# Performance work log

Hardware: AMD Instinct MI355X
Metric: run time of the kernel (lower is better)

## Reference

```python
import jax, jax.numpy as jnp
import numpy as np

B = 4096
D = 68 * 68  # 4624
L = 68
E = 1024


def setup_inputs() -> dict:
    key = jax.random.key(0)
    ks = jax.random.split(key, 24)
    rn = lambda k, shape, scale: jax.random.normal(k, shape, dtype=jnp.float32) * scale
    inp = {
        "x": rn(ks[0], (B, D), 1.0),
        "eps": rn(ks[1], (B, L), 1.0),
        # weights scaled ~1/sqrt(fan_in) to avoid sigmoid saturation
        "fc11_w": rn(ks[2], (E, D), 1.0 / np.sqrt(D)),
        "fc11_b": rn(ks[3], (E,), 0.01),
        "fc12_w": rn(ks[4], (E, D), 1.0 / np.sqrt(D)),
        "fc12_b": rn(ks[5], (E,), 0.01),
        "fc21_w": rn(ks[6], (L, E), 1.0 / np.sqrt(E)),
        "fc21_b": rn(ks[7], (L,), 0.01),
        "fc22_w": rn(ks[8], (L, E), 1.0 / np.sqrt(E)),
        "fc22_b": rn(ks[9], (L,), 0.01),
        "W3": rn(ks[10], (5, L, L), 1.0 / np.sqrt(L)),
        "b3": rn(ks[11], (5, L), 0.01),
        "W4": rn(ks[12], (5, L, L), 1.0 / np.sqrt(L)),
        "b4": rn(ks[13], (5, L), 0.01),
        "W5": rn(ks[14], (3, L, L), 1.0 / np.sqrt(L)),
        "b5": rn(ks[15], (3, L), 0.01),
        "fc6_w": rn(ks[16], (D, D), 1.0 / np.sqrt(D)),
        "fc6_b": rn(ks[17], (D,), 0.01),
        "fcy_w": rn(ks[18], (1, L), 1.0 / np.sqrt(L)),
        "fcy_b": rn(ks[19], (1,), 0.01),
    }
    return inp


def _forward(x, eps, fc11_w, fc11_b, fc12_w, fc12_b, fc21_w, fc21_b,
             fc22_w, fc22_b, W3, b3, W4, b4, W5, b5, fc6_w, fc6_b, fcy_w, fcy_b):
    b = x.shape[0]
    # encode (dropout in eval mode -> identity)
    h11 = jax.nn.relu(x @ fc11_w.T + fc11_b)
    h12 = jax.nn.relu(x @ fc12_w.T + fc12_b)
    mu = h11 @ fc21_w.T + fc21_b          # [B, 68]
    logvar = h12 @ fc22_w.T + fc22_b      # [B, 68]
    # reparameterize
    z = mu + eps * jnp.exp(0.5 * logvar)
    y = mu @ fcy_w.T + fcy_b              # [B, 1]
    # decode: 5 parallel 68-dim branches (vectorized over branch axis k)
    h3 = jnp.einsum('bd,kod->kbo', z, W3) + b3[:, None, :]     # [5,B,68]
    # source: h31 has no sigmoid, h32..h35 do
    h3 = jnp.concatenate([h3[:1], jax.nn.sigmoid(h3[1:])], axis=0)
    h4 = jax.nn.sigmoid(jnp.einsum('kbd,kod->kbo', h3, W4) + b4[:, None, :])
    # source reuses fc53 for branches 4 and 5: weight index map [0,1,2,2,2]
    idx = jnp.array([0, 1, 2, 2, 2])
    h5 = jnp.einsum('kbd,kod->kbo', h4, W5[idx]) + b5[idx][:, None, :]  # [5,B,68]
    # source: h6 = h51 only (other branch outer-products are dead code)
    h51 = h5[0]                                                # [B,68]
    outer = (h51[:, :, None] * h51[:, None, :]).reshape(b, D)  # bmm outer product
    recon = jax.nn.sigmoid(outer @ fc6_w.T + fc6_b)            # [B, 4624]
    return recon, mu, logvar, y


def reference(x, eps, fc11_w, fc11_b, fc12_w, fc12_b, fc21_w, fc21_b,
              fc22_w, fc22_b, W3, b3, W4, b4, W5, b5, fc6_w, fc6_b, fcy_w, fcy_b):
    return _forward(x, eps, fc11_w, fc11_b, fc12_w, fc12_b, fc21_w, fc21_b,
                    fc22_w, fc22_b, W3, b3, W4, b4, W5, b5, fc6_w, fc6_b, fcy_w, fcy_b)
```

## Files before the change

### kernel.cpp

```cpp
#include <hip/hip_runtime.h>
#include <hip/hip_bf16.h>
#include <cstdint>
#include <cstddef>

typedef __bf16 bf16x8 __attribute__((ext_vector_type(8)));
typedef __bf16 bf16x4 __attribute__((ext_vector_type(4)));
typedef float  floatx4 __attribute__((ext_vector_type(4)));

#define DEV __device__ __forceinline__

DEV __bf16 f2b(float x) { return (__bf16)x; }

DEV void async_ld16(const void* g, void* l) {
    __builtin_amdgcn_global_load_lds(
        (const __attribute__((address_space(1))) unsigned int*)g,
        (__attribute__((address_space(3))) unsigned int*)l,
        16, 0, 0);
}

#define BATCH 4096
#define DDIM  4624
#define DPAD  4672
#define LDIM  68
#define EDIM  1024
#define N1    2048
#define KB    2048
#define N2PAD 4736
#define NPAIR 2346
#define K2PAD 2368

DEV void build_ptab(unsigned short* ptab, int t, int nthr) {
    for (int i = t; i < LDIM; i += nthr) {
        int p0 = i * (137 - i) / 2;
        for (int j = i; j < LDIM; ++j)
            ptab[p0 + (j - i)] = (unsigned short)((i << 8) | j);
    }
}

#define PREP_GRID 7880
__global__ __launch_bounds__(256) void prep(
        const float* __restrict__ x, const float* __restrict__ w11,
        const float* __restrict__ w12, const float* __restrict__ w21,
        const float* __restrict__ w22, const float* __restrict__ w6,
        __bf16* __restrict__ xb, __bf16* __restrict__ w1_pad,
        __bf16* __restrict__ w2_pad, __bf16* __restrict__ w6s) {
    __shared__ float rowbuf[DDIM];
    __shared__ unsigned short ptab[K2PAD];
    const int b = blockIdx.x;
    const int t = threadIdx.x;

    if (b < 3072) {
        const float* src;
        __bf16* dst;
        int rows, lb, vg;
        if (b < 2048)      { src = x;   dst = xb;                          rows = BATCH; lb = b;        vg = 2048; }
        else if (b < 2560) { src = w11; dst = w1_pad;                      rows = 1024;  lb = b - 2048; vg = 512; }
        else               { src = w12; dst = w1_pad + (size_t)1024 * DPAD; rows = 1024; lb = b - 2560; vg = 512; }
        const int gpr = DPAD / 4;
        const long total = (long)rows * gpr;
        for (long g = lb * 256L + t; g < total; g += vg * 256L) {
            int row = (int)(g / gpr);
            int c4  = (int)(g - (long)row * gpr) * 4;
            bf16x4 v;
            if (c4 < DDIM) {
                floatx4 f = *(const floatx4*)(src + (size_t)row * DDIM + c4);
                v[0] = f2b(f[0]); v[1] = f2b(f[1]); v[2] = f2b(f[2]); v[3] = f2b(f[3]);
            } else {
                v[0] = v[1] = v[2] = v[3] = (__bf16)0.0f;
            }
            *(bf16x4*)(dst + (size_t)row * DPAD + c4) = v;
        }
    } else if (b < 3144) {
        const int lb = b - 3072;
        const int total = 144 * 512;
        for (int g = lb * 256 + t; g < total; g += 72 * 256) {
            int row = g >> 9;
            int c4  = (g & 511) * 4;
            bf16x4 v;
            v[0] = v[1] = v[2] = v[3] = (__bf16)0.0f;
            if (row < 68 && c4 < 1024) {
                floatx4 f = *(const floatx4*)(w21 + (size_t)row * EDIM + c4);
                v[0] = f2b(f[0]); v[1] = f2b(f[1]); v[2] = f2b(f[2]); v[3] = f2b(f[3]);
            } else if (row >= 68 && row < 136 && c4 >= 1024) {
                floatx4 f = *(const floatx4*)(w22 + (size_t)(row - 68) * EDIM + (c4 - 1024));
                v[0] = f2b(f[0]); v[1] = f2b(f[1]); v[2] = f2b(f[2]); v[3] = f2b(f[3]);
            }
            *(bf16x4*)(w2_pad + (size_t)row * KB + c4) = v;
        }
    } else {
        const int o = b - 3144;
        if (o < DDIM) {
            const float* src = w6 + (size_t)o * DDIM;
            for (int idx = t; idx < DDIM / 4; idx += 256)
                *(floatx4*)(rowbuf + idx * 4) = *(const floatx4*)(src + idx * 4);
        }
        build_ptab(ptab, t, 256);
        __syncthreads();
        for (int p4 = t; p4 < K2PAD / 4; p4 += 256) {
            bf16x4 v;
#pragma unroll
            for (int u = 0; u < 4; ++u) {
                int p = p4 * 4 + u;
                float val = 0.f;
                if (o < DDIM && p < NPAIR) {
                    int ij = ptab[p];
                    int i = ij >> 8, j = ij & 255;
                    val = (i == j) ? rowbuf[i * LDIM + i]
                                   : (rowbuf[i * LDIM + j] + rowbuf[j * LDIM + i]);
                }
                v[u] = f2b(val);
            }
            *(bf16x4*)(w6s + (size_t)o * K2PAD + p4 * 4) = v;
        }
    }
}

template <int EPI>
__launch_bounds__(256, 2)
__global__ void gemm_bt(const __bf16* __restrict__ A, int lda,
                        const __bf16* __restrict__ W, int ldb, int KT,
                        __bf16* __restrict__ outb, float* __restrict__ outf, int ldc,
                        const float* __restrict__ bias0, const float* __restrict__ bias1) {
    __shared__ __align__(16) __bf16 smA[128 * 64];
    __shared__ __align__(16) __bf16 smB[128 * 64];

    const int t  = threadIdx.x;
    const int l  = t & 63;
    const int w  = t >> 6;
    const int m0 = blockIdx.x * 128;
    const int n0 = blockIdx.y * 128;
    const int wm = (w & 1) * 64;
    const int wn = (w >> 1) * 64;

    const int srow   = t >> 3;
    const int schunk = (t & 7) ^ (srow & 7);
    const __bf16* pa = A + (size_t)(m0 + srow) * lda + schunk * 8;
    const __bf16* pb = W + (size_t)(n0 + srow) * ldb + schunk * 8;
    char* dA = (char*)smA + t * 16;
    char* dB = (char*)smB + t * 16;

    floatx4 acc[4][4];
#pragma unroll
    for (int mi = 0; mi < 4; ++mi)
#pragma unroll
        for (int ni = 0; ni < 4; ++ni) {
            floatx4 z = {0.f, 0.f, 0.f, 0.f};
            acc[mi][ni] = z;
        }

    for (int kt = 0; kt < KT; ++kt) {
#pragma unroll
        for (int i = 0; i < 4; ++i) {
            async_ld16(pa + (size_t)i * 32 * lda, dA + i * 4096);
            async_ld16(pb + (size_t)i * 32 * ldb, dB + i * 4096);
        }
        pa += 64; pb += 64;
        __syncthreads();

#pragma unroll
        for (int h = 0; h < 2; ++h) {
            bf16x8 af[4], bfr[4];
#pragma unroll
            for (int mi = 0; mi < 4; ++mi) {
                int r = wm + mi * 16 + (l & 15);
                int c = ((h << 2) | (l >> 4)) ^ (r & 7);
                af[mi] = *(const bf16x8*)((const char*)smA + r * 128 + c * 16);
            }
#pragma unroll
            for (int ni = 0; ni < 4; ++ni) {
                int r = wn + ni * 16 + (l & 15);
                int c = ((h << 2) | (l >> 4)) ^ (r & 7);
                bfr[ni] = *(const bf16x8*)((const char*)smB + r * 128 + c * 16);
            }
#pragma unroll
            for (int mi = 0; mi < 4; ++mi)
#pragma unroll
                for (int ni = 0; ni < 4; ++ni)
                    acc[mi][ni] = __builtin_amdgcn_mfma_f32_16x16x32_bf16(af[mi], bfr[ni],
                                                                         acc[mi][ni], 0, 0, 0);
        }
        __syncthreads();
    }

    const int colbase = n0 + wn + (l & 15);
    const int rowbase = m0 + wm + (l >> 4) * 4;
#pragma unroll
    for (int ni = 0; ni < 4; ++ni) {
        int col = colbase + ni * 16;
        if (EPI == 1 && col >= DDIM) continue;
        float bias = (EPI == 0)
                         ? ((col < 1024) ? bias0[col] : bias1[col - 1024])
                         : bias0[col];
#pragma unroll
        for (int mi = 0; mi < 4; ++mi) {
            int row = rowbase + mi * 16;
#pragma unroll
            for (int r = 0; r < 4; ++r) {
                float v = acc[mi][ni][r] + bias;
                if (EPI == 0) {
                    v = v > 0.f ? v : 0.f;
                    outb[(size_t)(row + r) * ldc + col] = f2b(v);
                } else {
                    v = 1.f / (1.f + __expf(-v));
                    outf[(size_t)(row + r) * ldc + col] = v;
                }
            }
        }
    }
}

__launch_bounds__(64, 4)
__global__ void gemmB(const __bf16* __restrict__ h, const __bf16* __restrict__ w2,
                      float* __restrict__ muvar) {
    const int l    = threadIdx.x;
    const int m0   = blockIdx.x * 16;
    const int k0   = blockIdx.y * 512;
    const int row  = l & 15;
    const int quad = l >> 4;
    float* mv = muvar + (size_t)blockIdx.y * BATCH * 136;

    floatx4 acc[9];
#pragma unroll
    for (int ni = 0; ni < 9; ++ni) {
        floatx4 z = {0.f, 0.f, 0.f, 0.f};
        acc[ni] = z;
    }

    const __bf16* ap = h + (size_t)(m0 + row) * KB + k0 + quad * 8;
    for (int kt = 0; kt < 16; ++kt) {
        bf16x8 a = *(const bf16x8*)ap;
        ap += 32;
#pragma unroll
        for (int ni = 0; ni < 9; ++ni) {
            const __bf16* bp = w2 + (size_t)(ni * 16 + row) * KB + k0 + kt * 32 + quad * 8;
            bf16x8 b = *(const bf16x8*)bp;
            acc[ni] = __builtin_amdgcn_mfma_f32_16x16x32_bf16(a, b, acc[ni], 0, 0, 0);
        }
    }
#pragma unroll
    for (int ni = 0; ni < 9; ++ni) {
        int col = ni * 16 + row;
        if (col < 136) {
#pragma unroll
            for (int r = 0; r < 4; ++r) {
                int orow = m0 + quad * 4 + r;
                mv[(size_t)orow * 136 + col] = acc[ni][r];
            }
        }
    }
}

__global__ void decode(const float* __restrict__ muvar, const float* __restrict__ eps,
                       const float* __restrict__ b21, const float* __restrict__ b22,
                       const float* __restrict__ W3, const float* __restrict__ b3,
                       const float* __restrict__ W4, const float* __restrict__ b4,
                       const float* __restrict__ W5, const float* __restrict__ b5,
                       const float* __restrict__ fcyw, const float* __restrict__ fcyb,
                       float* __restrict__ out_mu, float* __restrict__ out_lv,
                       float* __restrict__ out_y, __bf16* __restrict__ A2) {
    __shared__ float w3s[DDIM], w4s[DDIM], w5s[DDIM];
    __shared__ float b3s[LDIM], b4s[LDIM], b5s[LDIM], fys[LDIM];
    __shared__ float zb[16][LDIM], h3b[16][LDIM], h51b[16][LDIM], mub[16][LDIM];
    __shared__ unsigned short ptab[K2PAD];

    const int t  = threadIdx.x;
    const int r0 = blockIdx.x * 16;

    for (int i = t; i < DDIM; i += 256) {
        w3s[i] = W3[i];
        w4s[i] = W4[i];
        w5s[i] = W5[i];
    }
    if (t < LDIM) {
        b3s[t] = b3[t];
        b4s[t] = b4[t];
        b5s[t] = b5[t];
        fys[t] = fcyw[t];
    }
    build_ptab(ptab, t, 256);
    __syncthreads();

    for (int idx = t; idx < 16 * LDIM; idx += 256) {
        int r = idx / LDIM, o = idx - r * LDIM;
        int row = r0 + r;
        float mu = b21[o];
        float lv = b22[o];
#pragma unroll
        for (int s = 0; s < 4; ++s) {
            const float* mv = muvar + (size_t)s * BATCH * 136 + (size_t)row * 136;
            mu += mv[o];
            lv += mv[68 + o];
        }
        float z = mu + eps[(size_t)row * LDIM + o] * __expf(0.5f * lv);
        zb[r][o]  = z;
        mub[r][o] = mu;
        out_mu[(size_t)row * LDIM + o] = mu;
        out_lv[(size_t)row * LDIM + o] = lv;
    }
    __syncthreads();

    if (t < 16) {
        int row = r0 + t;
        float s = fcyb[0];
        for (int o = 0; o < LDIM; ++o)
            s += mub[t][o] * fys[o];
        out_y[row] = s;
    }

    for (int idx = t; idx < 16 * LDIM; idx += 256) {
        int r = idx / LDIM, o = idx - r * LDIM;
        float s = b3s[o];
        for (int d = 0; d < LDIM; ++d) s += zb[r][d] * w3s[o * LDIM + d];
        h3b[r][o] = s;
    }
    __syncthreads();

    for (int idx = t; idx < 16 * LDIM; idx += 256) {
        int r = idx / LDIM, o = idx - r * LDIM;
        float s = b4s[o];
        for (int d = 0; d < LDIM; ++d) s += h3b[r][d] * w4s[o * LDIM + d];
        zb[r][o] = 1.f / (1.f + __expf(-s));
    }
    __syncthreads();

    for (int idx = t; idx < 16 * LDIM; idx += 256) {
        int r = idx / LDIM, o = idx - r * LDIM;
        float s = b5s[o];
        for (int d = 0; d < LDIM; ++d) s += zb[r][d] * w5s[o * LDIM + d];
        h51b[r][o] = s;
    }
    __syncthreads();

    for (int idx = t; idx < 16 * (K2PAD / 4); idx += 256) {
        int r  = idx / (K2PAD / 4);
        int p4 = (idx - r * (K2PAD / 4)) * 4;
        int row = r0 + r;
        bf16x4 v;
#pragma unroll
        for (int u = 0; u < 4; ++u) {
            int p = p4 + u;
            float val = 0.f;
            if (p < NPAIR) {
                int ij = ptab[p];
                val = h51b[r][ij >> 8] * h51b[r][ij & 255];
            }
            v[u] = f2b(val);
        }
        *(bf16x4*)(A2 + (size_t)row * K2PAD + p4) = v;
    }
}

extern "C" void kernel_launch(void* const* d_in, const int* in_sizes, int n_in,
                              void* d_out, int out_size, void* d_ws, size_t ws_size,
                              hipStream_t stream) {
    const float* x    = (const float*)d_in[0];
    const float* eps  = (const float*)d_in[1];
    const float* w11  = (const float*)d_in[2];
    const float* b11  = (const float*)d_in[3];
    const float* w12  = (const float*)d_in[4];
    const float* b12  = (const float*)d_in[5];
    const float* w21  = (const float*)d_in[6];
    const float* b21  = (const float*)d_in[7];
    const float* w22  = (const float*)d_in[8];
    const float* b22  = (const float*)d_in[9];
    const float* W3   = (const float*)d_in[10];
    const float* b3   = (const float*)d_in[11];
    const float* W4   = (const float*)d_in[12];
    const float* b4   = (const float*)d_in[13];
    const float* W5   = (const float*)d_in[14];
    const float* b5   = (const float*)d_in[15];
    const float* w6   = (const float*)d_in[16];
    const float* b6   = (const float*)d_in[17];
    const float* fcyw = (const float*)d_in[18];
    const float* fcyb = (const float*)d_in[19];

    float* out       = (float*)d_out;
    float* out_recon = out;
    float* out_mu    = out + (size_t)BATCH * DDIM;
    float* out_lv    = out_mu + (size_t)BATCH * LDIM;
    float* out_y     = out_lv + (size_t)BATCH * LDIM;

    char* ws = (char*)d_ws;
    size_t off = 0;
    __bf16* xb     = (__bf16*)(ws + off); off += (size_t)BATCH * DPAD * 2;
    __bf16* w1_pad = (__bf16*)(ws + off); off += (size_t)N1 * DPAD * 2;
    __bf16* w6s    = (__bf16*)(ws + off); off += (size_t)N2PAD * K2PAD * 2;
    __bf16* hbuf   = (__bf16*)(ws + off); off += (size_t)BATCH * KB * 2;
    __bf16* w2_pad = (__bf16*)(ws + off); off += (size_t)144 * KB * 2;
    float*  muvar  = (float*) (ws + off); off += (size_t)4 * BATCH * 136 * 4;
    __bf16* A2     = (__bf16*)(ws + off);

    prep<<<PREP_GRID, 256, 0, stream>>>(x, w11, w12, w21, w22, w6,
                                        xb, w1_pad, w2_pad, w6s);

    gemm_bt<0><<<dim3(32, 16), 256, 0, stream>>>(
        xb, DPAD, w1_pad, DPAD, DPAD / 64, hbuf, nullptr, N1, b11, b12);

    gemmB<<<dim3(BATCH / 16, 4), 64, 0, stream>>>(hbuf, w2_pad, muvar);

    decode<<<BATCH / 16, 256, 0, stream>>>(muvar, eps, b21, b22, W3, b3, W4, b4, W5, b5,
                                           fcyw, fcyb, out_mu, out_lv, out_y, A2);

    gemm_bt<1><<<dim3(32, N2PAD / 128), 256, 0, stream>>>(
        A2, K2PAD, w6s, K2PAD, K2PAD / 64, nullptr, out_recon, DDIM, b6, nullptr);
}
```

Measured before the change: 524.1 us.

## Fuse mu/logvar GEMM into decode kernel and widen prep stores to 16 bytes

The separate gemmB kernel is merged into the decode kernel. Each of the four waves computes one K-quarter of the mu/logvar projection for the block's 16 rows and keeps the partial sums in shared memory, so the fp32 muvar round-trip through global memory and one kernel launch go away. The prep conversion loops now handle 8 elements per thread with bf16x8 stores instead of 4. The small decoder weight matrices are also padded to stride 69 in LDS to avoid bank conflicts. The fused kernel uses more shared memory (about 35 KB more for muv), which may lower occupancy of the decode stage.

```diff
diff --git a/kernel.cpp b/kernel.cpp
--- a/kernel.cpp
+++ b/kernel.cpp
@@ -22,6 +22,7 @@
 #define DDIM  4624
 #define DPAD  4672
 #define LDIM  68
+#define LPAD  69
 #define EDIM  1024
 #define N1    2048
 #define KB    2048
@@ -53,39 +54,50 @@
         const float* src;
         __bf16* dst;
         int rows, lb, vg;
-        if (b < 2048)      { src = x;   dst = xb;                          rows = BATCH; lb = b;        vg = 2048; }
-        else if (b < 2560) { src = w11; dst = w1_pad;                      rows = 1024;  lb = b - 2048; vg = 512; }
-        else               { src = w12; dst = w1_pad + (size_t)1024 * DPAD; rows = 1024; lb = b - 2560; vg = 512; }
-        const int gpr = DPAD / 4;
+        if (b < 2048)      { src = x;   dst = xb;                           rows = BATCH; lb = b;        vg = 2048; }
+        else if (b < 2560) { src = w11; dst = w1_pad;                       rows = 1024;  lb = b - 2048; vg = 512; }
+        else               { src = w12; dst = w1_pad + (size_t)1024 * DPAD; rows = 1024;  lb = b - 2560; vg = 512; }
+        const int gpr = DPAD / 8;
         const long total = (long)rows * gpr;
         for (long g = lb * 256L + t; g < total; g += vg * 256L) {
             int row = (int)(g / gpr);
-            int c4  = (int)(g - (long)row * gpr) * 4;
-            bf16x4 v;
-            if (c4 < DDIM) {
-                floatx4 f = *(const floatx4*)(src + (size_t)row * DDIM + c4);
-                v[0] = f2b(f[0]); v[1] = f2b(f[1]); v[2] = f2b(f[2]); v[3] = f2b(f[3]);
+            int c8  = (int)(g - (long)row * gpr) * 8;
+            bf16x8 v;
+            if (c8 < DDIM) {
+                const float* p = src + (size_t)row * DDIM + c8;
+                floatx4 f0 = *(const floatx4*)p;
+                floatx4 f1 = *(const floatx4*)(p + 4);
+                v[0] = f2b(f0[0]); v[1] = f2b(f0[1]); v[2] = f2b(f0[2]); v[3] = f2b(f0[3]);
+                v[4] = f2b(f1[0]); v[5] = f2b(f1[1]); v[6] = f2b(f1[2]); v[7] = f2b(f1[3]);
             } else {
-                v[0] = v[1] = v[2] = v[3] = (__bf16)0.0f;
-            }
-            *(bf16x4*)(dst + (size_t)row * DPAD + c4) = v;
+#pragma unroll
+                for (int u = 0; u < 8; ++u) v[u] = (__bf16)0.0f;
+            }
+            *(bf16x8*)(dst + (size_t)row * DPAD + c8) = v;
         }
     } else if (b < 3144) {
         const int lb = b - 3072;
-        const int total = 144 * 512;
+        const int total = 144 * 256;
         for (int g = lb * 256 + t; g < total; g += 72 * 256) {
-            int row = g >> 9;
-            int c4  = (g & 511) * 4;
-            bf16x4 v;
-            v[0] = v[1] = v[2] = v[3] = (__bf16)0.0f;
-            if (row < 68 && c4 < 1024) {
-                floatx4 f = *(const floatx4*)(w21 + (size_t)row * EDIM + c4);
-                v[0] = f2b(f[0]); v[1] = f2b(f[1]); v[2] = f2b(f[2]); v[3] = f2b(f[3]);
-            } else if (row >= 68 && row < 136 && c4 >= 1024) {
-                floatx4 f = *(const floatx4*)(w22 + (size_t)(row - 68) * EDIM + (c4 - 1024));
-                v[0] = f2b(f[0]); v[1] = f2b(f[1]); v[2] = f2b(f[2]); v[3] = f2b(f[3]);
-            }
-            *(bf16x4*)(w2_pad + (size_t)row * KB + c4) = v;
+            int row = g >> 8;
+            int c8  = (g & 255) * 8;
+            bf16x8 v;
+#pragma unroll
+            for (int u = 0; u < 8; ++u) v[u] = (__bf16)0.0f;
+            if (row < 68 && c8 < 1024) {
+                const float* p = w21 + (size_t)row * EDIM + c8;
+                floatx4 f0 = *(const floatx4*)p;
+                floatx4 f1 = *(const floatx4*)(p + 4);
+                v[0] = f2b(f0[0]); v[1] = f2b(f0[1]); v[2] = f2b(f0[2]); v[3] = f2b(f0[3]);
+                v[4] = f2b(f1[0]); v[5] = f2b(f1[1]); v[6] = f2b(f1[2]); v[7] = f2b(f1[3]);
+            } else if (row >= 68 && row < 136 && c8 >= 1024) {
+                const float* p = w22 + (size_t)(row - 68) * EDIM + (c8 - 1024);
+                floatx4 f0 = *(const floatx4*)p;
+                floatx4 f1 = *(const floatx4*)(p + 4);
+                v[0] = f2b(f0[0]); v[1] = f2b(f0[1]); v[2] = f2b(f0[2]); v[3] = f2b(f0[3]);
+                v[4] = f2b(f1[0]); v[5] = f2b(f1[1]); v[6] = f2b(f1[2]); v[7] = f2b(f1[3]);
+            }
+            *(bf16x8*)(w2_pad + (size_t)row * KB + c8) = v;
         }
     } else {
         const int o = b - 3144;
@@ -96,11 +108,11 @@
         }
         build_ptab(ptab, t, 256);
         __syncthreads();
-        for (int p4 = t; p4 < K2PAD / 4; p4 += 256) {
-            bf16x4 v;
-#pragma unroll
-            for (int u = 0; u < 4; ++u) {
-                int p = p4 * 4 + u;
+        for (int p8 = t; p8 < K2PAD / 8; p8 += 256) {
+            bf16x8 v;
+#pragma unroll
+            for (int u = 0; u < 8; ++u) {
+                int p = p8 * 8 + u;
                 float val = 0.f;
                 if (o < DDIM && p < NPAIR) {
                     int ij = ptab[p];
@@ -110,7 +122,7 @@
                 }
                 v[u] = f2b(val);
             }
-            *(bf16x4*)(w6s + (size_t)o * K2PAD + p4 * 4) = v;
+            *(bf16x8*)(w6s + (size_t)o * K2PAD + p8 * 8) = v;
         }
     }
 }
@@ -209,67 +221,65 @@
     }
 }
 
-__launch_bounds__(64, 4)
-__global__ void gemmB(const __bf16* __restrict__ h, const __bf16* __restrict__ w2,
-                      float* __restrict__ muvar) {
-    const int l    = threadIdx.x;
-    const int m0   = blockIdx.x * 16;
-    const int k0   = blockIdx.y * 512;
-    const int row  = l & 15;
-    const int quad = l >> 4;
-    float* mv = muvar + (size_t)blockIdx.y * BATCH * 136;
-
-    floatx4 acc[9];
-#pragma unroll
-    for (int ni = 0; ni < 9; ++ni) {
-        floatx4 z = {0.f, 0.f, 0.f, 0.f};
-        acc[ni] = z;
-    }
-
-    const __bf16* ap = h + (size_t)(m0 + row) * KB + k0 + quad * 8;
-    for (int kt = 0; kt < 16; ++kt) {
-        bf16x8 a = *(const bf16x8*)ap;
-        ap += 32;
-#pragma unroll
-        for (int ni = 0; ni < 9; ++ni) {
-            const __bf16* bp = w2 + (size_t)(ni * 16 + row) * KB + k0 + kt * 32 + quad * 8;
-            bf16x8 b = *(const bf16x8*)bp;
-            acc[ni] = __builtin_amdgcn_mfma_f32_16x16x32_bf16(a, b, acc[ni], 0, 0, 0);
-        }
-    }
-#pragma unroll
-    for (int ni = 0; ni < 9; ++ni) {
-        int col = ni * 16 + row;
-        if (col < 136) {
-#pragma unroll
-            for (int r = 0; r < 4; ++r) {
-                int orow = m0 + quad * 4 + r;
-                mv[(size_t)orow * 136 + col] = acc[ni][r];
-            }
-        }
-    }
-}
-
-__global__ void decode(const float* __restrict__ muvar, const float* __restrict__ eps,
-                       const float* __restrict__ b21, const float* __restrict__ b22,
-                       const float* __restrict__ W3, const float* __restrict__ b3,
-                       const float* __restrict__ W4, const float* __restrict__ b4,
-                       const float* __restrict__ W5, const float* __restrict__ b5,
-                       const float* __restrict__ fcyw, const float* __restrict__ fcyb,
-                       float* __restrict__ out_mu, float* __restrict__ out_lv,
-                       float* __restrict__ out_y, __bf16* __restrict__ A2) {
-    __shared__ float w3s[DDIM], w4s[DDIM], w5s[DDIM];
+__global__ __launch_bounds__(256) void decode_f(
+        const __bf16* __restrict__ h, const __bf16* __restrict__ w2,
+        const float* __restrict__ eps,
+        const float* __restrict__ b21, const float* __restrict__ b22,
+        const float* __restrict__ W3, const float* __restrict__ b3,
+        const float* __restrict__ W4, const float* __restrict__ b4,
+        const float* __restrict__ W5, const float* __restrict__ b5,
+        const float* __restrict__ fcyw, const float* __restrict__ fcyb,
+        float* __restrict__ out_mu, float* __restrict__ out_lv,
+        float* __restrict__ out_y, __bf16* __restrict__ A2) {
+    __shared__ float muv[4][16][136];
+    __shared__ float w3s[LDIM * LPAD], w4s[LDIM * LPAD], w5s[LDIM * LPAD];
     __shared__ float b3s[LDIM], b4s[LDIM], b5s[LDIM], fys[LDIM];
     __shared__ float zb[16][LDIM], h3b[16][LDIM], h51b[16][LDIM], mub[16][LDIM];
     __shared__ unsigned short ptab[K2PAD];
 
     const int t  = threadIdx.x;
+    const int l  = t & 63;
+    const int w  = t >> 6;
     const int r0 = blockIdx.x * 16;
 
+    {
+        const int row  = l & 15;
+        const int quad = l >> 4;
+        const int k0   = w * 512;
+        floatx4 acc[9];
+#pragma unroll
+        for (int ni = 0; ni < 9; ++ni) {
+            floatx4 z = {0.f, 0.f, 0.f, 0.f};
+            acc[ni] = z;
+        }
+        const __bf16* ap = h + (size_t)(r0 + row) * KB + k0 + quad * 8;
+        for (int kt = 0; kt < 16; ++kt) {
+            bf16x8 a = *(const bf16x8*)ap;
+            ap += 32;
+#pragma unroll
+            for (int ni = 0; ni < 9; ++ni) {
+                const __bf16* bp = w2 + (size_t)(ni * 16 + row) * KB + k0 + kt * 32 + quad * 8;
+                bf16x8 b = *(const bf16x8*)bp;
+                acc[ni] = __builtin_amdgcn_mfma_f32_16x16x32_bf16(a, b, acc[ni], 0, 0, 0);
+            }
+        }
+#pragma unroll
+        for (int ni = 0; ni < 9; ++ni) {
+            int col = ni * 16 + row;
+            if (col < 136) {
+#pragma unroll
+                for (int r = 0; r < 4; ++r)
+                    muv[w][quad * 4 + r][col] = acc[ni][r];
+            }
+        }
+    }
+
     for (int i = t; i < DDIM; i += 256) {
-        w3s[i] = W3[i];
-        w4s[i] = W4[i];
-        w5s[i] = W5[i];
+        int o = i / LDIM, d = i - o * LDIM;
+        int dst = o * LPAD + d;
+        w3s[dst] = W3[i];
+        w4s[dst] = W4[i];
+        w5s[dst] = W5[i];
     }
     if (t < LDIM) {
         b3s[t] = b3[t];
@@ -283,14 +293,9 @@
     for (int idx = t; idx < 16 * LDIM; idx += 256) {
         int r = idx / LDIM, o = idx - r * LDIM;
         int row = r0 + r;
-        float mu = b21[o];
-        float lv = b22[o];
-#pragma unroll
-        for (int s = 0; s < 4; ++s) {
-            const float* mv = muvar + (size_t)s * BATCH * 136 + (size_t)row * 136;
-            mu += mv[o];
-            lv += mv[68 + o];
-        }
+        float mu = b21[o] + muv[0][r][o] + muv[1][r][o] + muv[2][r][o] + muv[3][r][o];
+        float lv = b22[o] + muv[0][r][68 + o] + muv[1][r][68 + o]
+                          + muv[2][r][68 + o] + muv[3][r][68 + o];
         float z = mu + eps[(size_t)row * LDIM + o] * __expf(0.5f * lv);
         zb[r][o]  = z;
         mub[r][o] = mu;
@@ -310,7 +315,7 @@
     for (int idx = t; idx < 16 * LDIM; idx += 256) {
         int r = idx / LDIM, o = idx - r * LDIM;
         float s = b3s[o];
-        for (int d = 0; d < LDIM; ++d) s += zb[r][d] * w3s[o * LDIM + d];
+        for (int d = 0; d < LDIM; ++d) s += zb[r][d] * w3s[o * LPAD + d];
         h3b[r][o] = s;
     }
     __syncthreads();
@@ -318,7 +323,7 @@
     for (int idx = t; idx < 16 * LDIM; idx += 256) {
         int r = idx / LDIM, o = idx - r * LDIM;
         float s = b4s[o];
-        for (int d = 0; d < LDIM; ++d) s += h3b[r][d] * w4s[o * LDIM + d];
+        for (int d = 0; d < LDIM; ++d) s += h3b[r][d] * w4s[o * LPAD + d];
         zb[r][o] = 1.f / (1.f + __expf(-s));
     }
     __syncthreads();
@@ -326,7 +331,7 @@
     for (int idx = t; idx < 16 * LDIM; idx += 256) {
         int r = idx / LDIM, o = idx - r * LDIM;
         float s = b5s[o];
-        for (int d = 0; d < LDIM; ++d) s += zb[r][d] * w5s[o * LDIM + d];
+        for (int d = 0; d < LDIM; ++d) s += zb[r][d] * w5s[o * LPAD + d];
         h51b[r][o] = s;
     }
     __syncthreads();
@@ -387,7 +392,6 @@
     __bf16* w6s    = (__bf16*)(ws + off); off += (size_t)N2PAD * K2PAD * 2;
     __bf16* hbuf   = (__bf16*)(ws + off); off += (size_t)BATCH * KB * 2;
     __bf16* w2_pad = (__bf16*)(ws + off); off += (size_t)144 * KB * 2;
-    float*  muvar  = (float*) (ws + off); off += (size_t)4 * BATCH * 136 * 4;
     __bf16* A2     = (__bf16*)(ws + off);
 
     prep<<<PREP_GRID, 256, 0, stream>>>(x, w11, w12, w21, w22, w6,
@@ -396,10 +400,9 @@
     gemm_bt<0><<<dim3(32, 16), 256, 0, stream>>>(
         xb, DPAD, w1_pad, DPAD, DPAD / 64, hbuf, nullptr, N1, b11, b12);
 
-    gemmB<<<dim3(BATCH / 16, 4), 64, 0, stream>>>(hbuf, w2_pad, muvar);
-
-    decode<<<BATCH / 16, 256, 0, stream>>>(muvar, eps, b21, b22, W3, b3, W4, b4, W5, b5,
-                                           fcyw, fcyb, out_mu, out_lv, out_y, A2);
+    decode_f<<<BATCH / 16, 256, 0, stream>>>(hbuf, w2_pad, eps, b21, b22, W3, b3,
+                                             W4, b4, W5, b5, fcyw, fcyb,
+                                             out_mu, out_lv, out_y, A2);
 
     gemm_bt<1><<<dim3(32, N2PAD / 128), 256, 0, stream>>>(
         A2, K2PAD, w6s, K2PAD, K2PAD / 64, nullptr, out_recon, DDIM, b6, nullptr);
```

New measurement: 517.5 us. Within noise of the previous version (-1.3%).
